# Performance work log

Measured on AMD Instinct MI355X. Metric: run time of the kernel, lower is better.

The kernel has to match this reference:

```python
import jax, jax.numpy as jnp
import numpy as np

TOP_K = 5
TRUNC = 100
EPS = 1e-07
B, T_STEPS, I_DIM, H_DIM, N_CLS = 32, 384, 64, 128, 10


def setup_inputs() -> dict:
    key = jax.random.key(0)
    ks = jax.random.split(key, 8)
    s = 1.0 / np.sqrt(H_DIM)
    u = lambda k, sh: jax.random.uniform(k, sh, jnp.float32, -s, s)
    return {
        "x": jax.random.normal(ks[0], (B, T_STEPS, I_DIM), jnp.float32),
        "W_ih": u(ks[1], (4 * H_DIM, I_DIM)),
        "W_hh": u(ks[2], (4 * H_DIM, H_DIM)),
        "b_ih": u(ks[3], (4 * H_DIM,)),
        "b_hh": u(ks[4], (4 * H_DIM,)),
        "w_t": jax.random.normal(ks[5], (2 * H_DIM, 1), jnp.float32) * 0.01,
        "W_fc": u(ks[6], (N_CLS, 2 * H_DIM)),
        "b_fc": u(ks[7], (N_CLS,)),
    }


def _lstm_cell(x_t, h, c, W_ih, W_hh, b_ih, b_hh):
    # torch.nn.LSTMCell: gate order i, f, g, o
    g = x_t @ W_ih.T + b_ih + h @ W_hh.T + b_hh
    i, f, gg, o = jnp.split(g, 4, axis=1)
    c = jax.nn.sigmoid(f) * c + jax.nn.sigmoid(i) * jnp.tanh(gg)
    h = jax.nn.sigmoid(o) * jnp.tanh(c)
    return h, c


def _sparse_attn(scores, mask, r):
    # scores: [B, T+1]; mask: valid-prefix bool [T+1]; r: traced valid length
    Bsz, L = scores.shape
    neg = jnp.where(mask[None, :], scores, -jnp.inf)

    def small(_):
        return jax.nn.softmax(neg, axis=1)

    def big(_):
        delta = jax.lax.top_k(neg, TOP_K)[0][:, -1] + EPS  # [B], k-th largest
        # faithful to torch: delta.repeat((1, r)).view(B, r) -> delta[(b*r+t) % B]
        dmat = delta[(jnp.arange(Bsz)[:, None] * r + jnp.arange(L)[None, :]) % Bsz]
        w = jnp.clip(scores - dmat, 0.0, None) * mask[None, :]
        return w / (jnp.sum(w, axis=1, keepdims=True) + EPS)

    return jax.lax.cond(r <= TOP_K, small, big, None)


def reference(x, W_ih, W_hh, b_ih, b_hh, w_t, W_fc, b_fc):
    Bsz, T, _ = x.shape
    H = W_hh.shape[1]
    dt = x.dtype
    buf0 = jnp.zeros((Bsz, T + 1, H), dt)  # h_old buffer; slot 0 (zeros) is valid
    pos = jnp.arange(T + 1)

    def step(carry, inp):
        h, c, buf = carry
        i, x_t = inp
        h, c = jax.lax.cond(
            (i + 1) % TRUNC == 0,
            lambda hc: (jax.lax.stop_gradient(hc[0]), jax.lax.stop_gradient(hc[1])),
            lambda hc: hc,
            (h, c),
        )
        h, c = _lstm_cell(x_t, h, c, W_ih, W_hh, b_ih, b_hh)
        r = i + 1  # remember_size (valid prefix of buf)
        mask = (pos < r).astype(dt)  # [T+1]
        mlp = jnp.tanh(jnp.concatenate(
            (jnp.broadcast_to(h[:, None, :], buf.shape), buf), axis=2))  # [B,T+1,2H]
        scores = (mlp @ w_t)[..., 0]  # [B, T+1]
        attn = _sparse_attn(scores, mask, r)  # [B, T+1], zero on invalid slots
        attn_c = jnp.einsum('bt,bth->bh', attn, buf)
        h = h + attn_c
        buf = jax.lax.dynamic_update_slice(buf, h[:, None, :], (0, r, 0))
        return (h, c, buf), (h, attn_c)

    init = (jnp.zeros((Bsz, H), dt), jnp.zeros((Bsz, H), dt), buf0)
    _, (hs, attn_all) = jax.lax.scan(step, init, (jnp.arange(T), jnp.swapaxes(x, 0, 1)))
    outputs = jnp.concatenate(
        (jnp.swapaxes(hs, 0, 1), jnp.swapaxes(attn_all, 0, 1)), axis=2)  # [B,T,2H]
    out = outputs @ W_fc.T + b_fc  # [B, T, num_classes]
    return out, jnp.swapaxes(hs, 0, 1)
```

## Files before the change

kernel.cpp:

```cpp
#include <hip/hip_runtime.h>
#include <stdint.h>

typedef unsigned long long u64;

#define NB   32
#define TST  384
#define IDM  64
#define HDM  128
#define NCLS 10
#define EPSF 1e-7f
#define LOG2E 1.44269504088896340736f

#define O_SBUF 0
#define O_WLDS 388
#define O_ACT  776
#define O_GEX  968
#define O_RED  1480
#define O_DELT 2504
#define O_WFC  2536
#define O_BFC  5176
#define O_MISC 5188
#define SMTOT  5220

__device__ __forceinline__ float sigm(float x) {
  return 1.0f / (1.0f + __builtin_amdgcn_exp2f(-LOG2E * x));
}
__device__ __forceinline__ float tanh_f(float x) {
  return 1.0f - 2.0f / (1.0f + __builtin_amdgcn_exp2f(2.0f * LOG2E * x));
}

template <int CTRL>
__device__ __forceinline__ float dppadd(float v) {
  int t = __builtin_amdgcn_update_dpp(0, __builtin_bit_cast(int, v), CTRL, 0xF, 0xF, true);
  return v + __builtin_bit_cast(float, t);
}
__device__ __forceinline__ float sum8(float v) {
  v = dppadd<0xB1>(v);
  v = dppadd<0x4E>(v);
  v = dppadd<0x141>(v);
  return v;
}
__device__ __forceinline__ float sum16(float v) {
  v = dppadd<0xB1>(v);
  v = dppadd<0x4E>(v);
  v = dppadd<0x141>(v);
  v = dppadd<0x140>(v);
  return v;
}
__device__ __forceinline__ float wave_sum(float v) {
  v = sum16(v);
  v += __shfl_xor(v, 16, 64);
  v += __shfl_xor(v, 32, 64);
  return v;
}

__device__ __forceinline__ void mail_store(u64* p, u64 v) {
  asm volatile("global_store_dwordx2 %0, %1, off sc0 sc1"
               :: "v"(p), "v"(v) : "memory");
}
__device__ __forceinline__ u64 mail_load(u64* p) {
  u64 v;
  asm volatile("global_load_dwordx2 %0, %1, off sc0 sc1\n\t"
               "s_waitcnt vmcnt(0)"
               : "=v"(v) : "v"(p) : "memory");
  return v;
}

__global__ __launch_bounds__(512, 2)
void sab_kernel(const float* __restrict__ x, const float* __restrict__ Wih,
                const float* __restrict__ Whh, const float* __restrict__ bihp,
                const float* __restrict__ bhhp, const float* __restrict__ wtp,
                const float* __restrict__ Wfcp, const float* __restrict__ bfcp,
                float* __restrict__ dout, u64* __restrict__ mail) {
  __shared__ __align__(16) float SM[SMTOT];
  int* IMISC = (int*)(SM + O_MISC);
  int* IDX   = (int*)(SM + O_GEX);

  const int tid  = threadIdx.x;
  const int lane = tid & 63;
  const int wvid = tid >> 6;
  const int b    = blockIdx.x;
  const int go   = tid >> 3;
  const int kc   = tid & 7;

  float* hsout = dout + (size_t)NB * TST * NCLS;
  const float* myx = x + (size_t)b * TST * IDM;

  float w[8][24];
  #pragma unroll
  for (int i = 0; i < 8; ++i) {
    const int g = 8 * go + i;
    #pragma unroll
    for (int j = 0; j < 24; ++j) {
      const int k = 24 * kc + j;
      const float* sp = (k < IDM) ? (Wih + g * IDM + k) : (Whh + g * HDM + (k - IDM));
      w[i][j] = *sp;
    }
  }
  const float bias = bihp[tid] + bhhp[tid];

  float wt00 = 0.f, wt01 = 0.f, wt10 = 0.f, wt11 = 0.f;
  if (wvid == 0) {
    wt00 = wtp[lane];        wt01 = wtp[64 + lane];
    wt10 = wtp[128 + lane];  wt11 = wtp[192 + lane];
  }
  float cst0 = 0.f, cst1 = 0.f, hc0 = 0.f, hc1 = 0.f;

  float t5a = 0.f, t5b = -3e38f, t5c = -3e38f, t5d = -3e38f, t5e = -3e38f;

  for (int idx = tid; idx < NCLS * 256; idx += 512) {
    const int c = idx >> 8, k = idx & 255;
    SM[O_WFC + c * 264 + k] = Wfcp[idx];
  }
  if (tid < NCLS) SM[O_BFC + tid] = bfcp[tid];
  if (tid < HDM) SM[O_ACT + 64 + tid] = 0.f;
  if (tid < IDM) SM[O_ACT + tid] = myx[tid];
  if (tid == 0) {
    SM[O_SBUF] = 0.f;
    mail_store(&mail[b], 0ull);
    mail_store(&mail[NB + b], 0ull);
  }
  __syncthreads();

  for (int t = 0; t < TST; ++t) {
    const int r = t + 1;
    const bool big = (r > 5);

    float acc[8] = {0,0,0,0,0,0,0,0};
    {
      const float4* a4 = reinterpret_cast<const float4*>(SM + O_ACT + kc * 24);
      #pragma unroll
      for (int m = 0; m < 6; ++m) {
        const float4 av = a4[m];
        #pragma unroll
        for (int i = 0; i < 8; ++i) {
          acc[i] = fmaf(av.x, w[i][4*m+0], acc[i]);
          acc[i] = fmaf(av.y, w[i][4*m+1], acc[i]);
          acc[i] = fmaf(av.z, w[i][4*m+2], acc[i]);
          acc[i] = fmaf(av.w, w[i][4*m+3], acc[i]);
        }
      }
    }
    #pragma unroll
    for (int i = 0; i < 8; ++i) acc[i] = sum8(acc[i]);
    float pre = acc[0];
    #pragma unroll
    for (int i = 1; i < 8; ++i) if (kc == i) pre = acc[i];
    pre += bias;
    const bool tg = (tid >= 256) && (tid < 384);
    SM[O_RED + tid] = tg ? tanh_f(pre) : sigm(pre);
    __syncthreads();

    if (wvid == 0) {
      const float i0 = SM[O_RED + lane],        i1 = SM[O_RED + 64 + lane];
      const float f0 = SM[O_RED + 128 + lane],  f1 = SM[O_RED + 192 + lane];
      const float g0 = SM[O_RED + 256 + lane],  g1 = SM[O_RED + 320 + lane];
      const float o0 = SM[O_RED + 384 + lane],  o1 = SM[O_RED + 448 + lane];
      cst0 = f0 * cst0 + i0 * g0;
      cst1 = f1 * cst1 + i1 * g1;
      hc0  = o0 * tanh_f(cst0);
      hc1  = o1 * tanh_f(cst1);
      float th = tanh_f(hc0) * wt00 + tanh_f(hc1) * wt01;
      th = wave_sum(th);
      if (lane == 0) {
        SM[O_MISC] = th;
        if (big) {
          const u64 pv = (((u64)(unsigned)r) << 32) | (u64)__float_as_uint(t5e + th + EPSF);
          mail_store(&mail[(r & 1) * NB + b], pv);
        }
      }
    } else if (wvid == 7) {
      if (big && lane < NB) {
        u64* slot = &mail[(r & 1) * NB + lane];
        u64 v = mail_load(slot);
        while ((unsigned)(v >> 32) != (unsigned)r) v = mail_load(slot);
        SM[O_DELT + lane] = __uint_as_float((unsigned)v);
      }
    } else if (wvid == 1) {
      if (t + 1 < TST && lane < IDM)
        SM[O_ACT + lane] = myx[(size_t)(t + 1) * IDM + lane];
    } else if (t > 0 && tid < 288) {
      const int cls = (tid - 128) >> 4, p = tid & 15;
      float pt = 0.f;
      #pragma unroll
      for (int i = 0; i < 16; ++i) {
        const int k = p + 16 * i;
        pt = fmaf(SM[O_WFC + cls * 264 + k], SM[O_GEX + k], pt);
      }
      pt = sum16(pt);
      if (p == 0) dout[((size_t)(b * TST + (t - 1))) * NCLS + cls] = pt + SM[O_BFC + cls];
    }
    __syncthreads();

    const float s_h = SM[O_MISC];

    float wval = 0.f;
    bool pred = false;
    if (big) {
      if (tid < r) {
        const float sc = s_h + SM[O_SBUF + tid];
        wval = fmaxf(sc - SM[O_DELT + ((b * r + tid) & (NB - 1))], 0.f);
        SM[O_WLDS + tid] = wval;
        pred = (wval > 0.f) && (tid > 0);
      }
    } else {
      float scv = (tid < r) ? (s_h + SM[O_SBUF + tid]) : -3e38f;
      float mx = scv;
      #pragma unroll
      for (int s = 1; s < 64; s <<= 1) mx = fmaxf(mx, __shfl_xor(mx, s, 64));
      if (tid < r) {
        wval = __builtin_amdgcn_exp2f(LOG2E * (scv - mx));
        SM[O_WLDS + tid] = wval;
        pred = (tid > 0);
      }
    }
    const float wsp = wave_sum(wval);
    if (lane == 0) SM[O_MISC + 2 + wvid] = wsp;
    const u64 bmask = __ballot((int)pred);
    if (lane == 0) IMISC[16 + wvid] = (int)__popcll(bmask);
    __syncthreads();

    int wbase = 0, nnz = 0;
    #pragma unroll
    for (int i = 0; i < 8; ++i) {
      const int c = IMISC[16 + i];
      if (i < wvid) wbase += c;
      nnz += c;
    }
    if (pred) {
      const int pos = wbase + (int)__popcll(bmask & ((1ull << lane) - 1ull));
      IDX[pos] = tid;
    }
    __syncthreads();

    const int j8 = tid & 15, q = tid >> 4;
    float ac[8] = {0,0,0,0,0,0,0,0};
    for (int ii = q; ii < nnz; ii += 32) {
      const int tp = IDX[ii];
      const float wgt = SM[O_WLDS + tp];
      const float* bp = hsout + ((size_t)(b * TST + tp - 1)) * HDM + j8 * 8;
      const float4 v0 = *reinterpret_cast<const float4*>(bp);
      const float4 v1 = *reinterpret_cast<const float4*>(bp + 4);
      ac[0] = fmaf(wgt, v0.x, ac[0]); ac[1] = fmaf(wgt, v0.y, ac[1]);
      ac[2] = fmaf(wgt, v0.z, ac[2]); ac[3] = fmaf(wgt, v0.w, ac[3]);
      ac[4] = fmaf(wgt, v1.x, ac[4]); ac[5] = fmaf(wgt, v1.y, ac[5]);
      ac[6] = fmaf(wgt, v1.z, ac[6]); ac[7] = fmaf(wgt, v1.w, ac[7]);
    }
    #pragma unroll
    for (int i = 0; i < 8; ++i) {
      ac[i] += __shfl_xor(ac[i], 16, 64);
      ac[i] += __shfl_xor(ac[i], 32, 64);
    }
    if ((q & 3) == 0) {
      float4* r4 = reinterpret_cast<float4*>(SM + O_RED + wvid * 128 + j8 * 8);
      r4[0] = make_float4(ac[0], ac[1], ac[2], ac[3]);
      r4[1] = make_float4(ac[4], ac[5], ac[6], ac[7]);
    }
    __syncthreads();

    if (wvid == 0) {
      float wsum = 0.f;
      #pragma unroll
      for (int i = 0; i < 8; ++i) wsum += SM[O_MISC + 2 + i];
      const float inv = 1.0f / (wsum + (big ? EPSF : 0.f));
      float at0 = 0.f, at1 = 0.f;
      #pragma unroll
      for (int wv2 = 0; wv2 < 8; ++wv2) {
        at0 += SM[O_RED + wv2 * 128 + lane];
        at1 += SM[O_RED + wv2 * 128 + 64 + lane];
      }
      at0 *= inv; at1 *= inv;
      const float hf0 = hc0 + at0, hf1 = hc1 + at1;
      const size_t row = ((size_t)(b * TST + t)) * HDM;
      hsout[row + lane]      = hf0;
      hsout[row + 64 + lane] = hf1;
      SM[O_ACT + 64 + lane]  = hf0;
      SM[O_ACT + 128 + lane] = hf1;
      SM[O_GEX + lane]       = hf0;
      SM[O_GEX + 64 + lane]  = hf1;
      SM[O_GEX + 128 + lane] = at0;
      SM[O_GEX + 192 + lane] = at1;
      float tb = tanh_f(hf0) * wt10 + tanh_f(hf1) * wt11;
      tb = wave_sum(tb);
      if (lane == 0 && r < TST) {
        SM[O_SBUF + r] = tb;
        if (tb > t5e) {
          if (tb > t5a)      { t5e=t5d; t5d=t5c; t5c=t5b; t5b=t5a; t5a=tb; }
          else if (tb > t5b) { t5e=t5d; t5d=t5c; t5c=t5b; t5b=tb; }
          else if (tb > t5c) { t5e=t5d; t5d=t5c; t5c=tb; }
          else if (tb > t5d) { t5e=t5d; t5d=tb; }
          else               { t5e=tb; }
        }
      }
    }
    __syncthreads();
  }

  if (tid < 160) {
    const int cls = tid >> 4, p = tid & 15;
    float pt = 0.f;
    #pragma unroll
    for (int i = 0; i < 16; ++i) {
      const int k = p + 16 * i;
      pt = fmaf(SM[O_WFC + cls * 264 + k], SM[O_GEX + k], pt);
    }
    pt = sum16(pt);
    if (p == 0) dout[((size_t)(b * TST + (TST - 1))) * NCLS + cls] = pt + SM[O_BFC + cls];
  }
}

extern "C" void kernel_launch(void* const* d_in, const int* in_sizes, int n_in,
                              void* d_out, int out_size, void* d_ws, size_t ws_size,
                              hipStream_t stream) {
  const float* x   = (const float*)d_in[0];
  const float* Wih = (const float*)d_in[1];
  const float* Whh = (const float*)d_in[2];
  const float* bih = (const float*)d_in[3];
  const float* bhh = (const float*)d_in[4];
  const float* wt  = (const float*)d_in[5];
  const float* Wfc = (const float*)d_in[6];
  const float* bfc = (const float*)d_in[7];
  sab_kernel<<<dim3(NB), dim3(512), 0, stream>>>(
      x, Wih, Whh, bih, bhh, wt, Wfc, bfc, (float*)d_out, (u64*)d_ws);
}
```

Baseline: 1.920 ms.

## Replace LDS index compaction with per-wave ballot-driven gather of attended rows

The sparse attention gather used to build a compacted index list in LDS, which cost an extra barrier plus a prefix-count pass. Now each wave iterates its own ballot mask and broadcasts the weight with a shuffle. Each lane loads a float2 of the past hidden row, so one barrier per timestep is removed. Gate, h and w_t handling are remapped so each lane owns two adjacent hidden elements, and the FC input buffer is double-buffered by parity. The risk is that waves with many nonzero weights do the gather serially, one row at a time.

```diff
diff --git a/kernel.cpp b/kernel.cpp
--- a/kernel.cpp
+++ b/kernel.cpp
@@ -12,15 +12,14 @@
 #define LOG2E 1.44269504088896340736f
 
 #define O_SBUF 0
-#define O_WLDS 388
-#define O_ACT  776
-#define O_GEX  968
-#define O_RED  1480
-#define O_DELT 2504
-#define O_WFC  2536
-#define O_BFC  5176
-#define O_MISC 5188
-#define SMTOT  5220
+#define O_DELT 388
+#define O_MISC 420
+#define O_ACT  452
+#define O_GEX  644
+#define O_RED  1156
+#define O_WFC  2180
+#define O_BFC  4820
+#define SMTOT  4832
 
 __device__ __forceinline__ float sigm(float x) {
   return 1.0f / (1.0f + __builtin_amdgcn_exp2f(-LOG2E * x));
@@ -73,8 +72,6 @@
                 const float* __restrict__ Wfcp, const float* __restrict__ bfcp,
                 float* __restrict__ dout, u64* __restrict__ mail) {
   __shared__ __align__(16) float SM[SMTOT];
-  int* IMISC = (int*)(SM + O_MISC);
-  int* IDX   = (int*)(SM + O_GEX);
 
   const int tid  = threadIdx.x;
   const int lane = tid & 63;
@@ -99,10 +96,11 @@
   }
   const float bias = bihp[tid] + bhhp[tid];
 
-  float wt00 = 0.f, wt01 = 0.f, wt10 = 0.f, wt11 = 0.f;
+  float wt0a = 0.f, wt0b = 0.f, wt1a = 0.f, wt1b = 0.f;
   if (wvid == 0) {
-    wt00 = wtp[lane];        wt01 = wtp[64 + lane];
-    wt10 = wtp[128 + lane];  wt11 = wtp[192 + lane];
+    const float2 w0 = reinterpret_cast<const float2*>(wtp)[lane];
+    const float2 w1 = reinterpret_cast<const float2*>(wtp + HDM)[lane];
+    wt0a = w0.x; wt0b = w0.y; wt1a = w1.x; wt1b = w1.y;
   }
   float cst0 = 0.f, cst1 = 0.f, hc0 = 0.f, hc1 = 0.f;
 
@@ -125,6 +123,7 @@
   for (int t = 0; t < TST; ++t) {
     const int r = t + 1;
     const bool big = (r > 5);
+    const int par = t & 1;
 
     float acc[8] = {0,0,0,0,0,0,0,0};
     {
@@ -152,20 +151,19 @@
     __syncthreads();
 
     if (wvid == 0) {
-      const float i0 = SM[O_RED + lane],        i1 = SM[O_RED + 64 + lane];
-      const float f0 = SM[O_RED + 128 + lane],  f1 = SM[O_RED + 192 + lane];
-      const float g0 = SM[O_RED + 256 + lane],  g1 = SM[O_RED + 320 + lane];
-      const float o0 = SM[O_RED + 384 + lane],  o1 = SM[O_RED + 448 + lane];
-      cst0 = f0 * cst0 + i0 * g0;
-      cst1 = f1 * cst1 + i1 * g1;
-      hc0  = o0 * tanh_f(cst0);
-      hc1  = o1 * tanh_f(cst1);
-      float th = tanh_f(hc0) * wt00 + tanh_f(hc1) * wt01;
-      th = wave_sum(th);
+      const float2 gi  = *reinterpret_cast<const float2*>(SM + O_RED + 2 * lane);
+      const float2 gf  = *reinterpret_cast<const float2*>(SM + O_RED + 128 + 2 * lane);
+      const float2 gg  = *reinterpret_cast<const float2*>(SM + O_RED + 256 + 2 * lane);
+      const float2 go2 = *reinterpret_cast<const float2*>(SM + O_RED + 384 + 2 * lane);
+      cst0 = gf.x * cst0 + gi.x * gg.x;
+      cst1 = gf.y * cst1 + gi.y * gg.y;
+      hc0  = go2.x * tanh_f(cst0);
+      hc1  = go2.y * tanh_f(cst1);
+      const float sh = wave_sum(tanh_f(hc0) * wt0a + tanh_f(hc1) * wt0b);
       if (lane == 0) {
-        SM[O_MISC] = th;
+        SM[O_MISC] = sh;
         if (big) {
-          const u64 pv = (((u64)(unsigned)r) << 32) | (u64)__float_as_uint(t5e + th + EPSF);
+          const u64 pv = (((u64)(unsigned)r) << 32) | (u64)__float_as_uint(t5e + sh + EPSF);
           mail_store(&mail[(r & 1) * NB + b], pv);
         }
       }
@@ -176,16 +174,16 @@
         while ((unsigned)(v >> 32) != (unsigned)r) v = mail_load(slot);
         SM[O_DELT + lane] = __uint_as_float((unsigned)v);
       }
-    } else if (wvid == 1) {
-      if (t + 1 < TST && lane < IDM)
-        SM[O_ACT + lane] = myx[(size_t)(t + 1) * IDM + lane];
-    } else if (t > 0 && tid < 288) {
+    } else if (wvid == 6) {
+      if (t + 1 < TST) SM[O_ACT + lane] = myx[(size_t)(t + 1) * IDM + lane];
+    } else if (t > 0 && tid >= 128 && tid < 288) {
       const int cls = (tid - 128) >> 4, p = tid & 15;
+      const int gb = O_GEX + ((t - 1) & 1) * 256;
       float pt = 0.f;
       #pragma unroll
       for (int i = 0; i < 16; ++i) {
         const int k = p + 16 * i;
-        pt = fmaf(SM[O_WFC + cls * 264 + k], SM[O_GEX + k], pt);
+        pt = fmaf(SM[O_WFC + cls * 264 + k], SM[gb + k], pt);
       }
       pt = sum16(pt);
       if (p == 0) dout[((size_t)(b * TST + (t - 1))) * NCLS + cls] = pt + SM[O_BFC + cls];
@@ -193,97 +191,64 @@
     __syncthreads();
 
     const float s_h = SM[O_MISC];
-
+    const int tp = tid;
     float wval = 0.f;
     bool pred = false;
     if (big) {
-      if (tid < r) {
-        const float sc = s_h + SM[O_SBUF + tid];
-        wval = fmaxf(sc - SM[O_DELT + ((b * r + tid) & (NB - 1))], 0.f);
-        SM[O_WLDS + tid] = wval;
-        pred = (wval > 0.f) && (tid > 0);
+      if (tp < r) {
+        const float sc = s_h + SM[O_SBUF + tp];
+        wval = fmaxf(sc - SM[O_DELT + ((b * r + tp) & (NB - 1))], 0.f);
+        pred = (wval > 0.f) && (tp > 0);
       }
     } else {
-      float scv = (tid < r) ? (s_h + SM[O_SBUF + tid]) : -3e38f;
+      float scv = (tp < r) ? (s_h + SM[O_SBUF + tp]) : -3e38f;
       float mx = scv;
-      #pragma unroll
-      for (int s = 1; s < 64; s <<= 1) mx = fmaxf(mx, __shfl_xor(mx, s, 64));
-      if (tid < r) {
+      mx = fmaxf(mx, __shfl_xor(mx, 1, 64));  mx = fmaxf(mx, __shfl_xor(mx, 2, 64));
+      mx = fmaxf(mx, __shfl_xor(mx, 4, 64));  mx = fmaxf(mx, __shfl_xor(mx, 8, 64));
+      mx = fmaxf(mx, __shfl_xor(mx, 16, 64)); mx = fmaxf(mx, __shfl_xor(mx, 32, 64));
+      if (tp < r) {
         wval = __builtin_amdgcn_exp2f(LOG2E * (scv - mx));
-        SM[O_WLDS + tid] = wval;
-        pred = (tid > 0);
+        pred = (tp > 0);
       }
     }
     const float wsp = wave_sum(wval);
-    if (lane == 0) SM[O_MISC + 2 + wvid] = wsp;
-    const u64 bmask = __ballot((int)pred);
-    if (lane == 0) IMISC[16 + wvid] = (int)__popcll(bmask);
-    __syncthreads();
-
-    int wbase = 0, nnz = 0;
-    #pragma unroll
-    for (int i = 0; i < 8; ++i) {
-      const int c = IMISC[16 + i];
-      if (i < wvid) wbase += c;
-      nnz += c;
-    }
-    if (pred) {
-      const int pos = wbase + (int)__popcll(bmask & ((1ull << lane) - 1ull));
-      IDX[pos] = tid;
-    }
-    __syncthreads();
-
-    const int j8 = tid & 15, q = tid >> 4;
-    float ac[8] = {0,0,0,0,0,0,0,0};
-    for (int ii = q; ii < nnz; ii += 32) {
-      const int tp = IDX[ii];
-      const float wgt = SM[O_WLDS + tp];
-      const float* bp = hsout + ((size_t)(b * TST + tp - 1)) * HDM + j8 * 8;
-      const float4 v0 = *reinterpret_cast<const float4*>(bp);
-      const float4 v1 = *reinterpret_cast<const float4*>(bp + 4);
-      ac[0] = fmaf(wgt, v0.x, ac[0]); ac[1] = fmaf(wgt, v0.y, ac[1]);
-      ac[2] = fmaf(wgt, v0.z, ac[2]); ac[3] = fmaf(wgt, v0.w, ac[3]);
-      ac[4] = fmaf(wgt, v1.x, ac[4]); ac[5] = fmaf(wgt, v1.y, ac[5]);
-      ac[6] = fmaf(wgt, v1.z, ac[6]); ac[7] = fmaf(wgt, v1.w, ac[7]);
-    }
-    #pragma unroll
-    for (int i = 0; i < 8; ++i) {
-      ac[i] += __shfl_xor(ac[i], 16, 64);
-      ac[i] += __shfl_xor(ac[i], 32, 64);
-    }
-    if ((q & 3) == 0) {
-      float4* r4 = reinterpret_cast<float4*>(SM + O_RED + wvid * 128 + j8 * 8);
-      r4[0] = make_float4(ac[0], ac[1], ac[2], ac[3]);
-      r4[1] = make_float4(ac[4], ac[5], ac[6], ac[7]);
-    }
+    if (lane == 0) SM[O_MISC + 8 + wvid] = wsp;
+
+    float g0 = 0.f, g1 = 0.f;
+    u64 m = __ballot((int)pred);
+    while (m) {
+      const int l = __builtin_ctzll(m); m &= m - 1;
+      const float wgt = __shfl(wval, l, 64);
+      const int row = (wvid << 6) + l - 1;
+      const float2 v = reinterpret_cast<const float2*>(
+          hsout + (size_t)(b * TST + row) * HDM)[lane];
+      g0 = fmaf(wgt, v.x, g0);
+      g1 = fmaf(wgt, v.y, g1);
+    }
+    reinterpret_cast<float2*>(SM + O_RED + wvid * 128)[lane] = make_float2(g0, g1);
     __syncthreads();
 
     if (wvid == 0) {
       float wsum = 0.f;
       #pragma unroll
-      for (int i = 0; i < 8; ++i) wsum += SM[O_MISC + 2 + i];
-      const float inv = 1.0f / (wsum + (big ? EPSF : 0.f));
-      float at0 = 0.f, at1 = 0.f;
+      for (int i = 0; i < 8; ++i) wsum += SM[O_MISC + 8 + i];
+      const float inv = 1.0f / (wsum + (big ? EPSF : 0.0f));
+      float a0 = 0.f, a1 = 0.f;
       #pragma unroll
       for (int wv2 = 0; wv2 < 8; ++wv2) {
-        at0 += SM[O_RED + wv2 * 128 + lane];
-        at1 += SM[O_RED + wv2 * 128 + 64 + lane];
-      }
-      at0 *= inv; at1 *= inv;
+        const float2 p2 = reinterpret_cast<const float2*>(SM + O_RED + wv2 * 128)[lane];
+        a0 += p2.x; a1 += p2.y;
+      }
+      const float at0 = a0 * inv, at1 = a1 * inv;
       const float hf0 = hc0 + at0, hf1 = hc1 + at1;
-      const size_t row = ((size_t)(b * TST + t)) * HDM;
-      hsout[row + lane]      = hf0;
-      hsout[row + 64 + lane] = hf1;
-      SM[O_ACT + 64 + lane]  = hf0;
-      SM[O_ACT + 128 + lane] = hf1;
-      SM[O_GEX + lane]       = hf0;
-      SM[O_GEX + 64 + lane]  = hf1;
-      SM[O_GEX + 128 + lane] = at0;
-      SM[O_GEX + 192 + lane] = at1;
-      float tb = tanh_f(hf0) * wt10 + tanh_f(hf1) * wt11;
-      tb = wave_sum(tb);
-      if (lane == 0 && r < TST) {
-        SM[O_SBUF + r] = tb;
+      const float2 hv = make_float2(hf0, hf1);
+      reinterpret_cast<float2*>(hsout + (size_t)(b * TST + t) * HDM)[lane] = hv;
+      reinterpret_cast<float2*>(SM + O_ACT + 64)[lane] = hv;
+      reinterpret_cast<float2*>(SM + O_GEX + par * 256)[lane] = hv;
+      reinterpret_cast<float2*>(SM + O_GEX + par * 256 + 128)[lane] = make_float2(at0, at1);
+      if (r < TST) {
+        const float tb = wave_sum(tanh_f(hf0) * wt1a + tanh_f(hf1) * wt1b);
+        if (lane == 0) SM[O_SBUF + r] = tb;
         if (tb > t5e) {
           if (tb > t5a)      { t5e=t5d; t5d=t5c; t5c=t5b; t5b=t5a; t5a=tb; }
           else if (tb > t5b) { t5e=t5d; t5d=t5c; t5c=t5b; t5b=tb; }
@@ -298,11 +263,12 @@
 
   if (tid < 160) {
     const int cls = tid >> 4, p = tid & 15;
+    const int gb = O_GEX + ((TST - 1) & 1) * 256;
     float pt = 0.f;
     #pragma unroll
     for (int i = 0; i < 16; ++i) {
       const int k = p + 16 * i;
-      pt = fmaf(SM[O_WFC + cls * 264 + k], SM[O_GEX + k], pt);
+      pt = fmaf(SM[O_WFC + cls * 264 + k], SM[gb + k], pt);
     }
     pt = sum16(pt);
     if (p == 0) dout[((size_t)(b * TST + (TST - 1))) * NCLS + cls] = pt + SM[O_BFC + cls];
```

Result: slower. 3.259 ms (+69.7%).
